# Optimization experiments

Measured on AMD Instinct MI355X. Metric: run time of the kernel, lower is better.

Reference implementation:

```python
import jax, jax.numpy as jnp
import numpy as np

DIM = 64
HID = 128
DT_MAX = 0.1
BATCH = 16384


def _lin_init(k, fi, fo):
    kw, kb = jax.random.split(k)
    s = 1.0 / np.sqrt(fi)
    w = jax.random.uniform(kw, (fi, fo), minval=-s, maxval=s, dtype=jnp.float32)
    b = jax.random.uniform(kb, (fo,), minval=-s, maxval=s, dtype=jnp.float32)
    return w, b


def setup_inputs() -> dict:
    key = jax.random.key(0)
    ks = list(jax.random.split(key, 16))
    it = iter(ks)
    inp = {"z": jax.random.normal(next(it), (BATCH, DIM), dtype=jnp.float32)}
    layouts = [
        ("H", [(DIM, HID), (HID, HID), (HID, 1)]),
        ("D", [(DIM, HID), (HID, HID), (HID, 1)]),
        ("J", [(DIM, HID), (HID, DIM * DIM)]),
        ("B", [(DIM, HID), (HID, DIM * DIM)]),
        ("u", [(DIM, HID), (HID, DIM)]),
    ]
    for name, dims in layouts:
        for li, (fi, fo) in enumerate(dims, 1):
            w, b = _lin_init(next(it), fi, fo)
            inp[f"{name}w{li}"] = w
            inp[f"{name}b{li}"] = b
    inp["dt_logit"] = jnp.zeros((), dtype=jnp.float32)
    inp["energy_target"] = jnp.asarray(1.0, dtype=jnp.float32)
    return inp


def _scalar_net(z, w1, b1, w2, b2, w3, b3):
    # Linear->SiLU->Linear->SiLU->Linear, then softplus, squeeze -> [B]
    h = jax.nn.silu(z @ w1 + b1)
    h = jax.nn.silu(h @ w2 + b2)
    return jax.nn.softplus((h @ w3 + b3)[..., 0])


def reference(z, Hw1, Hb1, Hw2, Hb2, Hw3, Hb3,
              Dw1, Db1, Dw2, Db2, Dw3, Db3,
              Jw1, Jb1, Jw2, Jb2, Bw1, Bb1, Bw2, Bb2,
              uw1, ub1, uw2, ub2, dt_logit, energy_target):
    H = _scalar_net(z, Hw1, Hb1, Hw2, Hb2, Hw3, Hb3)  # [B]
    # autograd.grad(H.sum(), z) / grad(D.sum(), z)
    gH = jax.grad(lambda zz: _scalar_net(zz, Hw1, Hb1, Hw2, Hb2, Hw3, Hb3).sum())(z)
    gD = jax.grad(lambda zz: _scalar_net(zz, Dw1, Db1, Dw2, Db2, Dw3, Db3).sum())(z)
    # skew-symmetric J
    A = (jax.nn.silu(z @ Jw1 + Jb1) @ Jw2 + Jb2).reshape(-1, DIM, DIM)
    Jm = A - jnp.swapaxes(A, 1, 2)
    # PSD R = B B^T
    Bm = (jax.nn.silu(z @ Bw1 + Bb1) @ Bw2 + Bb2).reshape(-1, DIM, DIM)
    R = jnp.einsum('bik,bjk->bij', Bm, Bm)
    cons = jnp.einsum('bij,bj->bi', Jm, gH)
    diss = -jnp.einsum('bij,bj->bi', R, gD)
    u = jnp.tanh(z @ uw1 + ub1) @ uw2 + ub2
    pump = (energy_target - H)[:, None] * u
    dt = jax.nn.sigmoid(dt_logit) * DT_MAX
    dz = cons + diss + 0.1 * pump
    return z + dt * dz
```

## Files before the change

kernel.cpp:

```cpp
#include <hip/hip_runtime.h>

#define DIM 64
#define HID 128

typedef __attribute__((ext_vector_type(8))) short short8;
typedef __attribute__((ext_vector_type(4))) float f32x4;
typedef _Float16 h16x8 __attribute__((ext_vector_type(8)));
typedef _Float16 h16x2 __attribute__((ext_vector_type(2)));
typedef unsigned short ushort_t;

#define MFMA(A, B, C) __builtin_amdgcn_mfma_f32_16x16x32_bf16((A), (B), (C), 0, 0, 0)
#define MFMAH(A, B, C) __builtin_amdgcn_mfma_f32_16x16x32_f16((A), (B), (C), 0, 0, 0)

__device__ __forceinline__ float sigm(float x) { return 1.f / (1.f + __expf(-x)); }
__device__ __forceinline__ float siluf(float x) { return x * sigm(x); }
__device__ __forceinline__ float silup(float x) { float s = sigm(x); return s + x * s * (1.f - s); }
__device__ __forceinline__ float softplusf(float x) {
    if (x > 20.f) return x;
    return log1pf(__expf(x));
}
__device__ __forceinline__ ushort_t f2bf(float f) {
    union { float f; unsigned int u; } v; v.f = f;
    unsigned int r = v.u + 0x7fffu + ((v.u >> 16) & 1u);
    return (ushort_t)(r >> 16);
}
__device__ __forceinline__ ushort_t f2h(float f) {
    _Float16 h = (_Float16)f;
    union { _Float16 h; ushort_t u; } v; v.h = h; return v.u;
}
__device__ __forceinline__ _Float16 u2h(ushort_t u) {
    union { ushort_t u; _Float16 h; } v; v.u = u; return v.h;
}

#define OFF_HW1F  0
#define OFF_HW2F  8192
#define OFF_HW2TF 24576
#define OFF_HW1TF 40960
#define OFF_DW1F  49152
#define OFF_DW2F  57344
#define OFF_DW2TF 73728
#define OFF_DW1TF 90112
#define OFF_UW1F  98304
#define OFF_UW2F  106496
#define OFF_JW1F  114688
#define OFF_BW1F  122880

extern "C" __global__ __launch_bounds__(256)
void prep3_kernel(const float* __restrict__ Jw2, const float* __restrict__ Jb2,
                  const float* __restrict__ Bw2, const float* __restrict__ Bb2,
                  const float* __restrict__ Hw1, const float* __restrict__ Hw2,
                  const float* __restrict__ Dw1, const float* __restrict__ Dw2,
                  const float* __restrict__ uw1, const float* __restrict__ uw2,
                  const float* __restrict__ Jw1, const float* __restrict__ Bw1,
                  ushort_t* __restrict__ JW, ushort_t* __restrict__ BW1, ushort_t* __restrict__ BW2,
                  ushort_t* __restrict__ JbdF, ushort_t* __restrict__ Bb2F, ushort_t* __restrict__ Bb2TF,
                  ushort_t* __restrict__ SWF)
{
    const int b = blockIdx.x;
    if (b < 6144) {
        const int m = b >> 11;
        const int o = ((b & 2047) << 8) | threadIdx.x;
        const int e = o & 7, n = (o >> 3) & 63, g = (o >> 9) & 3, kt = o >> 11;
        const int k = (kt << 5) | (g << 3) | e;
        const int oi = k >> 7, h = k & 127;
        float val;
        if (m == 0)      val = Jw2[h * 4096 + n * 64 + oi] - Jw2[h * 4096 + oi * 64 + n];
        else if (m == 1) val = Bw2[h * 4096 + oi * 64 + n];
        else             val = Bw2[h * 4096 + n * 64 + oi];
        ushort_t* dst = (m == 0) ? JW : (m == 1) ? BW1 : BW2;
        dst[o] = f2h(val);
    } else if (b == 6144) {
        for (int e0 = threadIdx.x; e0 < 12288; e0 += 256) {
            const int m = e0 >> 12, o = e0 & 4095;
            const int e = o & 7, n = (o >> 3) & 63, g = (o >> 9) & 3, kb = o >> 11;
            const int k = (kb << 5) | (g << 3) | e;
            float val; ushort_t* dst;
            if (m == 0)      { val = Jb2[n * 64 + k] - Jb2[k * 64 + n]; dst = JbdF; }
            else if (m == 1) { val = Bb2[k * 64 + n];                   dst = Bb2F; }
            else             { val = Bb2[n * 64 + k];                   dst = Bb2TF; }
            dst[o] = f2h(val);
        }
    } else {
        const int e = (b - 6145) * 256 + threadIdx.x;
        float val = 0.f;
        if (e < 98304) {
            const int net = e / 49152;
            const int o = e - net * 49152;
            const float* W1s = net ? Dw1 : Hw1;
            const float* W2s = net ? Dw2 : Hw2;
            if (o < 8192) {
                int ks = o & 31, n = (o >> 5) & 127, kt = o >> 12;
                val = W1s[(kt * 32 + ks) * 128 + n];
            } else if (o < 24576) {
                int o2 = o - 8192;
                int ks = o2 & 31, n = (o2 >> 5) & 127, kt = o2 >> 12;
                val = W2s[(kt * 32 + ks) * 128 + n];
            } else if (o < 40960) {
                int o3 = o - 24576;
                int ks = o3 & 31, n = (o3 >> 5) & 127, kt = o3 >> 12;
                val = W2s[n * 128 + kt * 32 + ks];
            } else {
                int o4 = o - 40960;
                int ks = o4 & 31, n = (o4 >> 5) & 63, kt = o4 >> 11;
                val = W1s[n * 128 + kt * 32 + ks];
            }
        } else if (e < 106496) {
            int o = e - 98304;
            int ks = o & 31, n = (o >> 5) & 127, kt = o >> 12;
            val = uw1[(kt * 32 + ks) * 128 + n];
        } else if (e < 114688) {
            int o = e - 106496;
            int ks = o & 31, n = (o >> 5) & 63, kt = o >> 11;
            val = uw2[(kt * 32 + ks) * 64 + n];
        } else if (e < 122880) {
            int o = e - 114688;
            int ks = o & 31, n = (o >> 5) & 127, kt = o >> 12;
            val = Jw1[(kt * 32 + ks) * 128 + n];
        } else {
            int o = e - 122880;
            int ks = o & 31, n = (o >> 5) & 127, kt = o >> 12;
            val = Bw1[(kt * 32 + ks) * 128 + n];
        }
        SWF[e] = f2bf(val);
    }
}

__device__ __forceinline__ void scalar_net(
    int tid, int r0,
    const ushort_t* zbp, ushort_t* S1, ushort_t* S2, ushort_t* S3,
    float* yacc, float* srow, float* Hrow,
    const ushort_t* W1f, const ushort_t* W2f, const ushort_t* W2Tf, const ushort_t* W1Tf,
    const float* B1, const float* B2, const float* W3, const float* B3,
    ushort_t* gOut, int storeH)
{
    const int lane = tid & 63, w = tid >> 6;
    const int mt = w & 1, nh = w >> 1;
    const int cl = lane & 15, qq = lane >> 4;
    const int arow = mt * 16 + cl;
    const int crow = mt * 16 + qq * 4;

    {
        short8 a0 = *(const short8*)&zbp[arow * 72 + (qq << 3)];
        short8 a1 = *(const short8*)&zbp[arow * 72 + 32 + (qq << 3)];
        #pragma unroll
        for (int nt = 0; nt < 2; ++nt) {
            int n = nh * 32 + nt * 16 + cl;
            f32x4 acc = {0.f, 0.f, 0.f, 0.f};
            short8 b0 = *(const short8*)&W1f[(n << 5) + (qq << 3)];
            short8 b1 = *(const short8*)&W1f[((128 + n) << 5) + (qq << 3)];
            acc = MFMA(a0, b0, acc); acc = MFMA(a1, b1, acc);
            float bv = B1[n];
            #pragma unroll
            for (int q = 0; q < 4; ++q) {
                float aa = acc[q] + bv;
                S1[(crow + q) * 136 + n] = f2bf(siluf(aa));
                S2[(crow + q) * 136 + n] = f2bf(silup(aa));
            }
        }
    }
    __syncthreads();
    {
        short8 a[4];
        #pragma unroll
        for (int kt = 0; kt < 4; ++kt)
            a[kt] = *(const short8*)&S1[arow * 136 + kt * 32 + (qq << 3)];
        float yp[4] = {0.f, 0.f, 0.f, 0.f};
        #pragma unroll
        for (int nt = 0; nt < 2; ++nt) {
            int n = nh * 32 + nt * 16 + cl;
            f32x4 acc = {0.f, 0.f, 0.f, 0.f};
            #pragma unroll
            for (int kt = 0; kt < 4; ++kt) {
                short8 bb = *(const short8*)&W2f[((kt * 128 + n) << 5) + (qq << 3)];
                acc = MFMA(a[kt], bb, acc);
            }
            float bv = B2[n], w3v = W3[n];
            #pragma unroll
            for (int q = 0; q < 4; ++q) {
                float a2 = acc[q] + bv;
                yp[q] += siluf(a2) * w3v;
                S3[(crow + q) * 136 + n] = f2bf(w3v * silup(a2));
            }
        }
        #pragma unroll
        for (int q = 0; q < 4; ++q) {
            float p = yp[q];
            p += __shfl_xor(p, 1); p += __shfl_xor(p, 2);
            p += __shfl_xor(p, 4); p += __shfl_xor(p, 8);
            if (cl == 0) atomicAdd(&yacc[crow + q], p);
        }
    }
    __syncthreads();
    if (tid < 32) {
        float a3 = yacc[tid] + B3[0];
        srow[tid] = sigm(a3);
        if (storeH) Hrow[tid] = softplusf(a3);
        yacc[tid] = 0.f;
    }
    __syncthreads();
    {
        short8 a[4];
        #pragma unroll
        for (int kt = 0; kt < 4; ++kt)
            a[kt] = *(const short8*)&S3[arow * 136 + kt * 32 + (qq << 3)];
        #pragma unroll
        for (int nt = 0; nt < 2; ++nt) {
            int n = nh * 32 + nt * 16 + cl;
            f32x4 acc = {0.f, 0.f, 0.f, 0.f};
            #pragma unroll
            for (int kt = 0; kt < 4; ++kt) {
                short8 bb = *(const short8*)&W2Tf[((kt * 128 + n) << 5) + (qq << 3)];
                acc = MFMA(a[kt], bb, acc);
            }
            #pragma unroll
            for (int q = 0; q < 4; ++q) {
                float sp;
                { union { unsigned int u; float f; } v;
                  v.u = ((unsigned int)S2[(crow + q) * 136 + n]) << 16; sp = v.f; }
                S1[(crow + q) * 136 + n] = f2bf(acc[q] * sp);
            }
        }
    }
    __syncthreads();
    {
        short8 a[4];
        #pragma unroll
        for (int kt = 0; kt < 4; ++kt)
            a[kt] = *(const short8*)&S1[arow * 136 + kt * 32 + (qq << 3)];
        int n = nh * 16 + cl;
        f32x4 acc = {0.f, 0.f, 0.f, 0.f};
        #pragma unroll
        for (int kt = 0; kt < 4; ++kt) {
            short8 bb = *(const short8*)&W1Tf[((kt * 64 + n) << 5) + (qq << 3)];
            acc = MFMA(a[kt], bb, acc);
        }
        #pragma unroll
        for (int q = 0; q < 4; ++q) {
            int row = crow + q;
            gOut[(size_t)(r0 + row) * 64 + n] = f2h(srow[row] * acc[q]);
        }
    }
    __syncthreads();
}

extern "C" __global__ __launch_bounds__(512, 4)
void k1_kernel(const float* __restrict__ z,
               const float* __restrict__ Hb1, const float* __restrict__ Hb2,
               const float* __restrict__ Hw3, const float* __restrict__ Hb3,
               const float* __restrict__ Db1, const float* __restrict__ Db2,
               const float* __restrict__ Dw3, const float* __restrict__ Db3,
               const float* __restrict__ ub1, const float* __restrict__ ub2,
               const float* __restrict__ dtl, const float* __restrict__ etg,
               const ushort_t* __restrict__ SWF,
               ushort_t* __restrict__ gHbf, ushort_t* __restrict__ gDbf,
               float* __restrict__ out)
{
    __shared__ __align__(16) ushort_t zb[32][72];
    __shared__ __align__(16) ushort_t S1[32][136];
    __shared__ __align__(16) ushort_t S2[32][136];
    __shared__ __align__(16) ushort_t S3[32][136];
    __shared__ float yacc[32];
    __shared__ float srow[32];
    __shared__ float Hrow[32];

    const int tid = threadIdx.x;
    const int r0 = blockIdx.x * 32;

    {
        const float4* zg = (const float4*)(z + (size_t)r0 * 64);
        float4 v = zg[tid];
        int row = tid >> 4, c4 = (tid & 15) * 4;
        zb[row][c4 + 0] = f2bf(v.x); zb[row][c4 + 1] = f2bf(v.y);
        zb[row][c4 + 2] = f2bf(v.z); zb[row][c4 + 3] = f2bf(v.w);
        if (tid < 32) yacc[tid] = 0.f;
    }
    __syncthreads();

    scalar_net(tid, r0, &zb[0][0], &S1[0][0], &S2[0][0], &S3[0][0], yacc, srow, Hrow,
               SWF + OFF_HW1F, SWF + OFF_HW2F, SWF + OFF_HW2TF, SWF + OFF_HW1TF,
               Hb1, Hb2, Hw3, Hb3, gHbf, 1);
    scalar_net(tid, r0, &zb[0][0], &S1[0][0], &S2[0][0], &S3[0][0], yacc, srow, Hrow,
               SWF + OFF_DW1F, SWF + OFF_DW2F, SWF + OFF_DW2TF, SWF + OFF_DW1TF,
               Db1, Db2, Dw3, Db3, gDbf, 0);

    const int lane = tid & 63, w = tid >> 6;
    const int mt = w & 1, nh = w >> 1;
    const int cl = lane & 15, qq = lane >> 4;
    const int arow = mt * 16 + cl;
    const int crow = mt * 16 + qq * 4;

    {
        short8 a0 = *(const short8*)&zb[arow][(qq << 3)];
        short8 a1 = *(const short8*)&zb[arow][32 + (qq << 3)];
        const ushort_t* W1f = SWF + OFF_UW1F;
        #pragma unroll
        for (int nt = 0; nt < 2; ++nt) {
            int n = nh * 32 + nt * 16 + cl;
            f32x4 acc = {0.f, 0.f, 0.f, 0.f};
            short8 b0 = *(const short8*)&W1f[(n << 5) + (qq << 3)];
            short8 b1 = *(const short8*)&W1f[((128 + n) << 5) + (qq << 3)];
            acc = MFMA(a0, b0, acc); acc = MFMA(a1, b1, acc);
            float bv = ub1[n];
            #pragma unroll
            for (int q = 0; q < 4; ++q)
                S1[crow + q][n] = f2bf(tanhf(acc[q] + bv));
        }
    }
    __syncthreads();
    {
        short8 a[4];
        #pragma unroll
        for (int kt = 0; kt < 4; ++kt)
            a[kt] = *(const short8*)&S1[arow][kt * 32 + (qq << 3)];
        const ushort_t* W2f = SWF + OFF_UW2F;
        const float dtv = 0.1f * sigm(dtl[0]);
        const float et = etg[0];
        int n = nh * 16 + cl;
        f32x4 acc = {0.f, 0.f, 0.f, 0.f};
        #pragma unroll
        for (int kt = 0; kt < 4; ++kt) {
            short8 bb = *(const short8*)&W2f[((kt * 64 + n) << 5) + (qq << 3)];
            acc = MFMA(a[kt], bb, acc);
        }
        float bv = ub2[n];
        #pragma unroll
        for (int q = 0; q < 4; ++q) {
            int row = crow + q;
            size_t idx = (size_t)(r0 + row) * 64 + n;
            out[idx] = z[idx] + dtv * 0.1f * (et - Hrow[row]) * (acc[q] + bv);
        }
    }
}

#define LOADHF2H(SRC, HA, HB)                                                     \
    do {                                                                          \
        _Pragma("unroll")                                                         \
        for (int q4 = 0; q4 < 4; ++q4) {                                          \
            short8 sa = *(const short8*)&(SRC)[rr0][q4 * 32 + (qq << 3)];         \
            short8 sb = *(const short8*)&(SRC)[rr1][q4 * 32 + (qq << 3)];         \
            _Pragma("unroll")                                                     \
            for (int e = 0; e < 4; ++e) {                                         \
                h16x2 ta, tb;                                                     \
                ta[0] = u2h((ushort_t)sa[e * 2]); ta[1] = u2h((ushort_t)sa[e * 2 + 1]); \
                tb[0] = u2h((ushort_t)sb[e * 2]); tb[1] = u2h((ushort_t)sb[e * 2 + 1]); \
                (HA)[q4 * 4 + e] = ta;                                            \
                (HB)[q4 * 4 + e] = tb;                                            \
            }                                                                     \
        }                                                                         \
    } while (0)

#define HEAVY_PASS(Wbase, BFbase, G, HA, HB, A00, A01, A10, A11)                  \
    do {                                                                          \
        _Pragma("unroll 2")                                                       \
        for (int jj = 0; jj < 32; ++jj) {                                         \
            const int j = 2 * jj + ks;                                            \
            const ushort_t* bp = (Wbase) + (size_t)j * 8192 + (qq << 9);          \
            h16x8 bf0[4], bf1[4];                                                 \
            _Pragma("unroll")                                                     \
            for (int ki = 0; ki < 4; ++ki) {                                      \
                bf0[ki] = *(const h16x8*)&bp[ki * 2048 + col0 * 8];               \
                bf1[ki] = *(const h16x8*)&bp[ki * 2048 + col1 * 8];               \
            }                                                                     \
            _Float16 gA = u2h((G)[rr0][j]);                                       \
            _Float16 gB = u2h((G)[rr1][j]);                                       \
            h16x2 gA2; gA2[0] = gA; gA2[1] = gA;                                  \
            h16x2 gB2; gB2[0] = gB; gB2[1] = gB;                                  \
            _Pragma("unroll")                                                     \
            for (int ki = 0; ki < 4; ++ki) {                                      \
                union { h16x2 h2[4]; h16x8 v; } aA, aB;                           \
                _Pragma("unroll")                                                 \
                for (int e = 0; e < 4; ++e) {                                     \
                    aA.h2[e] = (HA)[ki * 4 + e] * gA2;                            \
                    aB.h2[e] = (HB)[ki * 4 + e] * gB2;                            \
                }                                                                 \
                A00 = MFMAH(aA.v, bf0[ki], A00); A01 = MFMAH(aA.v, bf1[ki], A01); \
                A10 = MFMAH(aB.v, bf0[ki], A10); A11 = MFMAH(aB.v, bf1[ki], A11); \
            }                                                                     \
        }                                                                         \
                             \
        {                                                                         \
            h16x8 abA = *(const h16x8*)&(G)[rr0][(ks << 5) + (qq << 3)];          \
            h16x8 abB = *(const h16x8*)&(G)[rr1][(ks << 5) + (qq << 3)];          \
            const ushort_t* bpb = (BFbase) + (ks << 11) + (qq << 9);              \
            h16x8 b0 = *(const h16x8*)&bpb[col0 * 8];                             \
            h16x8 b1 = *(const h16x8*)&bpb[col1 * 8];                             \
            A00 = MFMAH(abA, b0, A00); A01 = MFMAH(abA, b1, A01);                 \
            A10 = MFMAH(abB, b0, A10); A11 = MFMAH(abB, b1, A11);                 \
        }                                                                         \
                                             \
        __syncthreads();                                                          \
        if (ks == 1) {                                                            \
            _Pragma("unroll")                                                     \
            for (int q = 0; q < 4; ++q) {                                         \
                Pb[orow0 + q][col0] = A00[q]; Pb[orow0 + q][col1] = A01[q];       \
                Pb[orow1 + q][col0] = A10[q]; Pb[orow1 + q][col1] = A11[q];       \
            }                                                                     \
        }                                                                         \
        __syncthreads();                                                          \
        if (ks == 0) {                                                            \
            _Pragma("unroll")                                                     \
            for (int q = 0; q < 4; ++q) {                                         \
                A00[q] += Pb[orow0 + q][col0]; A01[q] += Pb[orow0 + q][col1];     \
                A10[q] += Pb[orow1 + q][col0]; A11[q] += Pb[orow1 + q][col1];     \
            }                                                                     \
        }                                                                         \
        __syncthreads();                                                          \
    } while (0)

extern "C" __global__ __launch_bounds__(256, 3)
void k2_kernel(const float* __restrict__ z,
               const float* __restrict__ Jb1, const float* __restrict__ Bb1,
               const float* __restrict__ dtl,
               const ushort_t* __restrict__ JW, const ushort_t* __restrict__ BW1,
               const ushort_t* __restrict__ BW2,
               const ushort_t* __restrict__ JbdF, const ushort_t* __restrict__ Bb2F,
               const ushort_t* __restrict__ Bb2TF,
               const ushort_t* __restrict__ SWF,
               const ushort_t* __restrict__ gHbf, const ushort_t* __restrict__ gDbf,
               float* __restrict__ out)
{
    __shared__ __align__(16) ushort_t zb[32][72];
    __shared__ __align__(16) ushort_t hJ2[32][136];
    __shared__ __align__(16) ushort_t hB2[32][136];
    __shared__ __align__(16) ushort_t gHb[32][72];
    __shared__ __align__(16) ushort_t gDb[32][72];
    __shared__ __align__(16) ushort_t vb2[32][72];
    __shared__ __align__(16) float Pb[32][68];

    const int tid = threadIdx.x;
    const int r0 = blockIdx.x * 32;

    {
        const float4* zg = (const float4*)(z + (size_t)r0 * 64);
        #pragma unroll
        for (int it = 0; it < 2; ++it) {
            int i = it * 256 + tid;
            float4 v = zg[i];
            int row = i >> 4, c4 = (i & 15) * 4;
            zb[row][c4 + 0] = f2bf(v.x); zb[row][c4 + 1] = f2bf(v.y);
            zb[row][c4 + 2] = f2bf(v.z); zb[row][c4 + 3] = f2bf(v.w);
        }
        const short8* gh = (const short8*)(gHbf + (size_t)r0 * 64);
        const short8* gd = (const short8*)(gDbf + (size_t)r0 * 64);
        int row = tid >> 3, s = tid & 7;
        *(short8*)&gHb[row][s * 8] = gh[tid];
        *(short8*)&gDb[row][s * 8] = gd[tid];
    }
    __syncthreads();

    const int lane = tid & 63, w = tid >> 6;
    const int cl = lane & 15, qq = lane >> 4;
    const int mt = w & 1, nh = w >> 1;
    const int arow = mt * 16 + cl;
    const int crowL = mt * 16 + qq * 4;

    {
        short8 a0 = *(const short8*)&zb[arow][(qq << 3)];
        short8 a1 = *(const short8*)&zb[arow][32 + (qq << 3)];
        const ushort_t* JW1f = SWF + OFF_JW1F;
        const ushort_t* BW1f = SWF + OFF_BW1F;
        #pragma unroll
        for (int nt = 0; nt < 4; ++nt) {
            int n = nh * 64 + nt * 16 + cl;
            f32x4 accJ = {0.f, 0.f, 0.f, 0.f}, accB = {0.f, 0.f, 0.f, 0.f};
            short8 jb0 = *(const short8*)&JW1f[(n << 5) + (qq << 3)];
            short8 jb1 = *(const short8*)&JW1f[((128 + n) << 5) + (qq << 3)];
            accJ = MFMA(a0, jb0, accJ); accJ = MFMA(a1, jb1, accJ);
            short8 bb0 = *(const short8*)&BW1f[(n << 5) + (qq << 3)];
            short8 bb1 = *(const short8*)&BW1f[((128 + n) << 5) + (qq << 3)];
            accB = MFMA(a0, bb0, accB); accB = MFMA(a1, bb1, accB);
            float jbv = Jb1[n], bbv = Bb1[n];
            #pragma unroll
            for (int q = 0; q < 4; ++q) {
                hJ2[crowL + q][n] = f2h(siluf(accJ[q] + jbv));
                hB2[crowL + q][n] = f2h(siluf(accB[q] + bbv));
            }
        }
    }
    __syncthreads();

    const int ch = w & 1;
    const int ks = w >> 1;
    const int rr0 = cl;
    const int rr1 = cl + 16;
    const int col0 = ch * 32 + cl;
    const int col1 = col0 + 16;
    const int orow0 = qq * 4;
    const int orow1 = orow0 + 16;

    h16x2 hfJA[16], hfJB[16], hfBA[16], hfBB[16];
    f32x4 c00 = {0,0,0,0}, c01 = {0,0,0,0}, c10 = {0,0,0,0}, c11 = {0,0,0,0};
    f32x4 v00 = {0,0,0,0}, v01 = {0,0,0,0}, v10 = {0,0,0,0}, v11 = {0,0,0,0};
    f32x4 d00 = {0,0,0,0}, d01 = {0,0,0,0}, d10 = {0,0,0,0}, d11 = {0,0,0,0};

    LOADHF2H(hJ2, hfJA, hfJB);
    HEAVY_PASS(JW, JbdF, gHb, hfJA, hfJB, c00, c01, c10, c11);

    LOADHF2H(hB2, hfBA, hfBB);
    HEAVY_PASS(BW1, Bb2F, gDb, hfBA, hfBB, v00, v01, v10, v11);

    if (ks == 0) {
        #pragma unroll
        for (int q = 0; q < 4; ++q) {
            vb2[orow0 + q][col0] = f2h(v00[q]); vb2[orow0 + q][col1] = f2h(v01[q]);
            vb2[orow1 + q][col0] = f2h(v10[q]); vb2[orow1 + q][col1] = f2h(v11[q]);
        }
    }
    __syncthreads();

    HEAVY_PASS(BW2, Bb2TF, vb2, hfBA, hfBB, d00, d01, d10, d11);

    if (ks == 0) {
        const float dtv = 0.1f * sigm(dtl[0]);
        #pragma unroll
        for (int q = 0; q < 4; ++q) {
            size_t i00 = (size_t)(r0 + orow0 + q) * 64 + col0;
            size_t i01 = (size_t)(r0 + orow0 + q) * 64 + col1;
            size_t i10 = (size_t)(r0 + orow1 + q) * 64 + col0;
            size_t i11 = (size_t)(r0 + orow1 + q) * 64 + col1;
            out[i00] += dtv * (c00[q] - d00[q]);
            out[i01] += dtv * (c01[q] - d01[q]);
            out[i10] += dtv * (c10[q] - d10[q]);
            out[i11] += dtv * (c11[q] - d11[q]);
        }
    }
}

extern "C" void kernel_launch(void* const* d_in, const int* in_sizes, int n_in,
                              void* d_out, int out_size, void* d_ws, size_t ws_size,
                              hipStream_t stream) {
    const float* p[27];
    for (int i = 0; i < 27; ++i) p[i] = (const float*)d_in[i];
    ushort_t* JW    = (ushort_t*)d_ws;
    ushort_t* BW1   = JW + 524288;
    ushort_t* BW2   = BW1 + 524288;
    ushort_t* JbdF  = BW2 + 524288;
    ushort_t* Bb2F  = JbdF + 4096;
    ushort_t* Bb2TF = Bb2F + 4096;
    ushort_t* gHbf  = Bb2TF + 4096;
    ushort_t* gDbf  = gHbf + (size_t)16384 * 64;
    ushort_t* SWF   = gDbf + (size_t)16384 * 64;

    hipLaunchKernelGGL(prep3_kernel, dim3(6657), dim3(256), 0, stream,
                       p[15], p[16], p[19], p[20],
                       p[1], p[3], p[7], p[9],
                       p[21], p[23], p[13], p[17],
                       JW, BW1, BW2, JbdF, Bb2F, Bb2TF, SWF);

    const int batch = in_sizes[0] / DIM;
    hipLaunchKernelGGL(k1_kernel, dim3(batch / 32), dim3(512), 0, stream,
                       p[0],
                       p[2], p[4], p[5], p[6],
                       p[8], p[10], p[11], p[12],
                       p[22], p[24],
                       p[25], p[26],
                       SWF, gHbf, gDbf, (float*)d_out);

    hipLaunchKernelGGL(k2_kernel, dim3(batch / 32), dim3(256), 0, stream,
                       p[0], p[14], p[18], p[25],
                       JW, BW1, BW2, JbdF, Bb2F, Bb2TF, SWF,
                       gHbf, gDbf, (float*)d_out);
}
```

Baseline: 110.1 us.

## Fuse scalar-net and heavy J/B kernels into one 512-thread kernel

Merges k1 (H/D gradient nets and pump term) and k2 (J/R matrix contractions) into a single kernel. gH and gD now stay in shared memory instead of round-tripping through global workspace, and the partial output is kept in a shared buffer rather than read back from global memory. The heavy pass now runs on 512 threads: the j loop is split across a new row-partition index, and partial sums are reduced with shared-memory atomicAdd in place of the two-phase Pb reduction. The cost is a much larger shared-memory footprint per block, which may lower occupancy, plus contention from the shared atomics.

```diff
diff --git a/kernel.cpp b/kernel.cpp
--- a/kernel.cpp
+++ b/kernel.cpp
@@ -126,12 +126,12 @@
 }
 
 __device__ __forceinline__ void scalar_net(
-    int tid, int r0,
+    int tid,
     const ushort_t* zbp, ushort_t* S1, ushort_t* S2, ushort_t* S3,
     float* yacc, float* srow, float* Hrow,
     const ushort_t* W1f, const ushort_t* W2f, const ushort_t* W2Tf, const ushort_t* W1Tf,
     const float* B1, const float* B2, const float* W3, const float* B3,
-    ushort_t* gOut, int storeH)
+    ushort_t* gL, int storeH)
 {
     const int lane = tid & 63, w = tid >> 6;
     const int mt = w & 1, nh = w >> 1;
@@ -237,99 +237,10 @@
         #pragma unroll
         for (int q = 0; q < 4; ++q) {
             int row = crow + q;
-            gOut[(size_t)(r0 + row) * 64 + n] = f2h(srow[row] * acc[q]);
-        }
-    }
-    __syncthreads();
-}
-
-extern "C" __global__ __launch_bounds__(512, 4)
-void k1_kernel(const float* __restrict__ z,
-               const float* __restrict__ Hb1, const float* __restrict__ Hb2,
-               const float* __restrict__ Hw3, const float* __restrict__ Hb3,
-               const float* __restrict__ Db1, const float* __restrict__ Db2,
-               const float* __restrict__ Dw3, const float* __restrict__ Db3,
-               const float* __restrict__ ub1, const float* __restrict__ ub2,
-               const float* __restrict__ dtl, const float* __restrict__ etg,
-               const ushort_t* __restrict__ SWF,
-               ushort_t* __restrict__ gHbf, ushort_t* __restrict__ gDbf,
-               float* __restrict__ out)
-{
-    __shared__ __align__(16) ushort_t zb[32][72];
-    __shared__ __align__(16) ushort_t S1[32][136];
-    __shared__ __align__(16) ushort_t S2[32][136];
-    __shared__ __align__(16) ushort_t S3[32][136];
-    __shared__ float yacc[32];
-    __shared__ float srow[32];
-    __shared__ float Hrow[32];
-
-    const int tid = threadIdx.x;
-    const int r0 = blockIdx.x * 32;
-
-    {
-        const float4* zg = (const float4*)(z + (size_t)r0 * 64);
-        float4 v = zg[tid];
-        int row = tid >> 4, c4 = (tid & 15) * 4;
-        zb[row][c4 + 0] = f2bf(v.x); zb[row][c4 + 1] = f2bf(v.y);
-        zb[row][c4 + 2] = f2bf(v.z); zb[row][c4 + 3] = f2bf(v.w);
-        if (tid < 32) yacc[tid] = 0.f;
-    }
-    __syncthreads();
-
-    scalar_net(tid, r0, &zb[0][0], &S1[0][0], &S2[0][0], &S3[0][0], yacc, srow, Hrow,
-               SWF + OFF_HW1F, SWF + OFF_HW2F, SWF + OFF_HW2TF, SWF + OFF_HW1TF,
-               Hb1, Hb2, Hw3, Hb3, gHbf, 1);
-    scalar_net(tid, r0, &zb[0][0], &S1[0][0], &S2[0][0], &S3[0][0], yacc, srow, Hrow,
-               SWF + OFF_DW1F, SWF + OFF_DW2F, SWF + OFF_DW2TF, SWF + OFF_DW1TF,
-               Db1, Db2, Dw3, Db3, gDbf, 0);
-
-    const int lane = tid & 63, w = tid >> 6;
-    const int mt = w & 1, nh = w >> 1;
-    const int cl = lane & 15, qq = lane >> 4;
-    const int arow = mt * 16 + cl;
-    const int crow = mt * 16 + qq * 4;
-
-    {
-        short8 a0 = *(const short8*)&zb[arow][(qq << 3)];
-        short8 a1 = *(const short8*)&zb[arow][32 + (qq << 3)];
-        const ushort_t* W1f = SWF + OFF_UW1F;
-        #pragma unroll
-        for (int nt = 0; nt < 2; ++nt) {
-            int n = nh * 32 + nt * 16 + cl;
-            f32x4 acc = {0.f, 0.f, 0.f, 0.f};
-            short8 b0 = *(const short8*)&W1f[(n << 5) + (qq << 3)];
-            short8 b1 = *(const short8*)&W1f[((128 + n) << 5) + (qq << 3)];
-            acc = MFMA(a0, b0, acc); acc = MFMA(a1, b1, acc);
-            float bv = ub1[n];
-            #pragma unroll
-            for (int q = 0; q < 4; ++q)
-                S1[crow + q][n] = f2bf(tanhf(acc[q] + bv));
-        }
-    }
-    __syncthreads();
-    {
-        short8 a[4];
-        #pragma unroll
-        for (int kt = 0; kt < 4; ++kt)
-            a[kt] = *(const short8*)&S1[arow][kt * 32 + (qq << 3)];
-        const ushort_t* W2f = SWF + OFF_UW2F;
-        const float dtv = 0.1f * sigm(dtl[0]);
-        const float et = etg[0];
-        int n = nh * 16 + cl;
-        f32x4 acc = {0.f, 0.f, 0.f, 0.f};
-        #pragma unroll
-        for (int kt = 0; kt < 4; ++kt) {
-            short8 bb = *(const short8*)&W2f[((kt * 64 + n) << 5) + (qq << 3)];
-            acc = MFMA(a[kt], bb, acc);
-        }
-        float bv = ub2[n];
-        #pragma unroll
-        for (int q = 0; q < 4; ++q) {
-            int row = crow + q;
-            size_t idx = (size_t)(r0 + row) * 64 + n;
-            out[idx] = z[idx] + dtv * 0.1f * (et - Hrow[row]) * (acc[q] + bv);
-        }
-    }
+            gL[row * 72 + n] = f2h(srow[row] * acc[q]);
+        }
+    }
+    __syncthreads();
 }
 
 #define LOADHF2H(SRC, HA, HB)                                                     \
@@ -349,11 +260,16 @@
         }                                                                         \
     } while (0)
 
-#define HEAVY_PASS(Wbase, BFbase, G, HA, HB, A00, A01, A10, A11)                  \
+#define HEAVY_PASS(Wbase, BFbase, HSRC, GS)                                       \
     do {                                                                          \
+        __syncthreads();                                                          \
+        for (int e2 = tid; e2 < 32 * 68; e2 += 512) (&Pb[0][0])[e2] = 0.f;        \
+        h16x2 hf0[16], hf1[16];                                                   \
+        LOADHF2H(HSRC, hf0, hf1);                                                 \
+        f32x4 A00 = {0,0,0,0}, A01 = {0,0,0,0}, A10 = {0,0,0,0}, A11 = {0,0,0,0}; \
         _Pragma("unroll 2")                                                       \
-        for (int jj = 0; jj < 32; ++jj) {                                         \
-            const int j = 2 * jj + ks;                                            \
+        for (int jj = 0; jj < 16; ++jj) {                                         \
+            const int j = (((rp << 4) + jj) << 1) + ks;                           \
             const ushort_t* bp = (Wbase) + (size_t)j * 8192 + (qq << 9);          \
             h16x8 bf0[4], bf1[4];                                                 \
             _Pragma("unroll")                                                     \
@@ -361,8 +277,8 @@
                 bf0[ki] = *(const h16x8*)&bp[ki * 2048 + col0 * 8];               \
                 bf1[ki] = *(const h16x8*)&bp[ki * 2048 + col1 * 8];               \
             }                                                                     \
-            _Float16 gA = u2h((G)[rr0][j]);                                       \
-            _Float16 gB = u2h((G)[rr1][j]);                                       \
+            _Float16 gA = u2h((GS)[rr0 * 72 + j]);                                \
+            _Float16 gB = u2h((GS)[rr1 * 72 + j]);                                \
             h16x2 gA2; gA2[0] = gA; gA2[1] = gA;                                  \
             h16x2 gB2; gB2[0] = gB; gB2[1] = gB;                                  \
             _Pragma("unroll")                                                     \
@@ -370,89 +286,131 @@
                 union { h16x2 h2[4]; h16x8 v; } aA, aB;                           \
                 _Pragma("unroll")                                                 \
                 for (int e = 0; e < 4; ++e) {                                     \
-                    aA.h2[e] = (HA)[ki * 4 + e] * gA2;                            \
-                    aB.h2[e] = (HB)[ki * 4 + e] * gB2;                            \
+                    aA.h2[e] = hf0[ki * 4 + e] * gA2;                             \
+                    aB.h2[e] = hf1[ki * 4 + e] * gB2;                             \
                 }                                                                 \
                 A00 = MFMAH(aA.v, bf0[ki], A00); A01 = MFMAH(aA.v, bf1[ki], A01); \
                 A10 = MFMAH(aB.v, bf0[ki], A10); A11 = MFMAH(aB.v, bf1[ki], A11); \
             }                                                                     \
         }                                                                         \
-                             \
-        {                                                                         \
-            h16x8 abA = *(const h16x8*)&(G)[rr0][(ks << 5) + (qq << 3)];          \
-            h16x8 abB = *(const h16x8*)&(G)[rr1][(ks << 5) + (qq << 3)];          \
+        if (rp == 0) {                                                            \
+            h16x8 abA = *(const h16x8*)&(GS)[rr0 * 72 + (ks << 5) + (qq << 3)];   \
+            h16x8 abB = *(const h16x8*)&(GS)[rr1 * 72 + (ks << 5) + (qq << 3)];   \
             const ushort_t* bpb = (BFbase) + (ks << 11) + (qq << 9);              \
             h16x8 b0 = *(const h16x8*)&bpb[col0 * 8];                             \
             h16x8 b1 = *(const h16x8*)&bpb[col1 * 8];                             \
             A00 = MFMAH(abA, b0, A00); A01 = MFMAH(abA, b1, A01);                 \
             A10 = MFMAH(abB, b0, A10); A11 = MFMAH(abB, b1, A11);                 \
         }                                                                         \
-                                             \
         __syncthreads();                                                          \
-        if (ks == 1) {                                                            \
-            _Pragma("unroll")                                                     \
-            for (int q = 0; q < 4; ++q) {                                         \
-                Pb[orow0 + q][col0] = A00[q]; Pb[orow0 + q][col1] = A01[q];       \
-                Pb[orow1 + q][col0] = A10[q]; Pb[orow1 + q][col1] = A11[q];       \
-            }                                                                     \
-        }                                                                         \
-        __syncthreads();                                                          \
-        if (ks == 0) {                                                            \
-            _Pragma("unroll")                                                     \
-            for (int q = 0; q < 4; ++q) {                                         \
-                A00[q] += Pb[orow0 + q][col0]; A01[q] += Pb[orow0 + q][col1];     \
-                A10[q] += Pb[orow1 + q][col0]; A11[q] += Pb[orow1 + q][col1];     \
-            }                                                                     \
+        _Pragma("unroll")                                                         \
+        for (int q = 0; q < 4; ++q) {                                             \
+            atomicAdd(&Pb[orow0 + q][col0], A00[q]);                              \
+            atomicAdd(&Pb[orow0 + q][col1], A01[q]);                              \
+            atomicAdd(&Pb[orow1 + q][col0], A10[q]);                              \
+            atomicAdd(&Pb[orow1 + q][col1], A11[q]);                              \
         }                                                                         \
         __syncthreads();                                                          \
     } while (0)
 
-extern "C" __global__ __launch_bounds__(256, 3)
-void k2_kernel(const float* __restrict__ z,
+extern "C" __global__ __launch_bounds__(512, 4)
+void kf_kernel(const float* __restrict__ z,
+               const float* __restrict__ Hb1, const float* __restrict__ Hb2,
+               const float* __restrict__ Hw3, const float* __restrict__ Hb3,
+               const float* __restrict__ Db1, const float* __restrict__ Db2,
+               const float* __restrict__ Dw3, const float* __restrict__ Db3,
+               const float* __restrict__ ub1, const float* __restrict__ ub2,
                const float* __restrict__ Jb1, const float* __restrict__ Bb1,
-               const float* __restrict__ dtl,
+               const float* __restrict__ dtl, const float* __restrict__ etg,
                const ushort_t* __restrict__ JW, const ushort_t* __restrict__ BW1,
                const ushort_t* __restrict__ BW2,
                const ushort_t* __restrict__ JbdF, const ushort_t* __restrict__ Bb2F,
                const ushort_t* __restrict__ Bb2TF,
                const ushort_t* __restrict__ SWF,
-               const ushort_t* __restrict__ gHbf, const ushort_t* __restrict__ gDbf,
                float* __restrict__ out)
 {
     __shared__ __align__(16) ushort_t zb[32][72];
+    __shared__ __align__(16) ushort_t S1[32][136];
+    __shared__ __align__(16) ushort_t S2[32][136];
+    __shared__ __align__(16) ushort_t S3[32][136];
+    __shared__ float yacc[32];
+    __shared__ float srow[32];
+    __shared__ float Hrow[32];
     __shared__ __align__(16) ushort_t hJ2[32][136];
     __shared__ __align__(16) ushort_t hB2[32][136];
     __shared__ __align__(16) ushort_t gHb[32][72];
     __shared__ __align__(16) ushort_t gDb[32][72];
     __shared__ __align__(16) ushort_t vb2[32][72];
     __shared__ __align__(16) float Pb[32][68];
+    __shared__ __align__(16) float baseb[32][64];
 
     const int tid = threadIdx.x;
     const int r0 = blockIdx.x * 32;
+    const float dtv = 0.1f * sigm(dtl[0]);
 
     {
         const float4* zg = (const float4*)(z + (size_t)r0 * 64);
-        #pragma unroll
-        for (int it = 0; it < 2; ++it) {
-            int i = it * 256 + tid;
-            float4 v = zg[i];
-            int row = i >> 4, c4 = (i & 15) * 4;
-            zb[row][c4 + 0] = f2bf(v.x); zb[row][c4 + 1] = f2bf(v.y);
-            zb[row][c4 + 2] = f2bf(v.z); zb[row][c4 + 3] = f2bf(v.w);
-        }
-        const short8* gh = (const short8*)(gHbf + (size_t)r0 * 64);
-        const short8* gd = (const short8*)(gDbf + (size_t)r0 * 64);
-        int row = tid >> 3, s = tid & 7;
-        *(short8*)&gHb[row][s * 8] = gh[tid];
-        *(short8*)&gDb[row][s * 8] = gd[tid];
-    }
-    __syncthreads();
+        float4 v = zg[tid];
+        int row = tid >> 4, c4 = (tid & 15) * 4;
+        zb[row][c4 + 0] = f2bf(v.x); zb[row][c4 + 1] = f2bf(v.y);
+        zb[row][c4 + 2] = f2bf(v.z); zb[row][c4 + 3] = f2bf(v.w);
+        if (tid < 32) yacc[tid] = 0.f;
+    }
+    __syncthreads();
+
+    scalar_net(tid, &zb[0][0], &S1[0][0], &S2[0][0], &S3[0][0], yacc, srow, Hrow,
+               SWF + OFF_HW1F, SWF + OFF_HW2F, SWF + OFF_HW2TF, SWF + OFF_HW1TF,
+               Hb1, Hb2, Hw3, Hb3, &gHb[0][0], 1);
+    scalar_net(tid, &zb[0][0], &S1[0][0], &S2[0][0], &S3[0][0], yacc, srow, Hrow,
+               SWF + OFF_DW1F, SWF + OFF_DW2F, SWF + OFF_DW2TF, SWF + OFF_DW1TF,
+               Db1, Db2, Dw3, Db3, &gDb[0][0], 0);
 
     const int lane = tid & 63, w = tid >> 6;
+    const int mt = w & 1, nh = w >> 1;
     const int cl = lane & 15, qq = lane >> 4;
-    const int mt = w & 1, nh = w >> 1;
     const int arow = mt * 16 + cl;
-    const int crowL = mt * 16 + qq * 4;
+    const int crow = mt * 16 + qq * 4;
+
+    {
+        short8 a0 = *(const short8*)&zb[arow][(qq << 3)];
+        short8 a1 = *(const short8*)&zb[arow][32 + (qq << 3)];
+        const ushort_t* W1f = SWF + OFF_UW1F;
+        #pragma unroll
+        for (int nt = 0; nt < 2; ++nt) {
+            int n = nh * 32 + nt * 16 + cl;
+            f32x4 acc = {0.f, 0.f, 0.f, 0.f};
+            short8 b0 = *(const short8*)&W1f[(n << 5) + (qq << 3)];
+            short8 b1 = *(const short8*)&W1f[((128 + n) << 5) + (qq << 3)];
+            acc = MFMA(a0, b0, acc); acc = MFMA(a1, b1, acc);
+            float bv = ub1[n];
+            #pragma unroll
+            for (int q = 0; q < 4; ++q)
+                S1[crow + q][n] = f2bf(tanhf(acc[q] + bv));
+        }
+    }
+    __syncthreads();
+    {
+        short8 a[4];
+        #pragma unroll
+        for (int kt = 0; kt < 4; ++kt)
+            a[kt] = *(const short8*)&S1[arow][kt * 32 + (qq << 3)];
+        const ushort_t* W2f = SWF + OFF_UW2F;
+        const float et = etg[0];
+        int n = nh * 16 + cl;
+        f32x4 acc = {0.f, 0.f, 0.f, 0.f};
+        #pragma unroll
+        for (int kt = 0; kt < 4; ++kt) {
+            short8 bb = *(const short8*)&W2f[((kt * 64 + n) << 5) + (qq << 3)];
+            acc = MFMA(a[kt], bb, acc);
+        }
+        float bv = ub2[n];
+        #pragma unroll
+        for (int q = 0; q < 4; ++q) {
+            int row = crow + q;
+            baseb[row][n] = z[(size_t)(r0 + row) * 64 + n]
+                          + dtv * 0.1f * (et - Hrow[row]) * (acc[q] + bv);
+        }
+    }
 
     {
         short8 a0 = *(const short8*)&zb[arow][(qq << 3)];
@@ -460,8 +418,8 @@
         const ushort_t* JW1f = SWF + OFF_JW1F;
         const ushort_t* BW1f = SWF + OFF_BW1F;
         #pragma unroll
-        for (int nt = 0; nt < 4; ++nt) {
-            int n = nh * 64 + nt * 16 + cl;
+        for (int nt = 0; nt < 2; ++nt) {
+            int n = nh * 32 + nt * 16 + cl;
             f32x4 accJ = {0.f, 0.f, 0.f, 0.f}, accB = {0.f, 0.f, 0.f, 0.f};
             short8 jb0 = *(const short8*)&JW1f[(n << 5) + (qq << 3)];
             short8 jb1 = *(const short8*)&JW1f[((128 + n) << 5) + (qq << 3)];
@@ -472,15 +430,16 @@
             float jbv = Jb1[n], bbv = Bb1[n];
             #pragma unroll
             for (int q = 0; q < 4; ++q) {
-                hJ2[crowL + q][n] = f2h(siluf(accJ[q] + jbv));
-                hB2[crowL + q][n] = f2h(siluf(accB[q] + bbv));
+                hJ2[crow + q][n] = f2h(siluf(accJ[q] + jbv));
+                hB2[crow + q][n] = f2h(siluf(accB[q] + bbv));
             }
         }
     }
     __syncthreads();
 
     const int ch = w & 1;
-    const int ks = w >> 1;
+    const int ks = (w >> 1) & 1;
+    const int rp = w >> 2;
     const int rr0 = cl;
     const int rr1 = cl + 16;
     const int col0 = ch * 32 + cl;
@@ -488,41 +447,22 @@
     const int orow0 = qq * 4;
     const int orow1 = orow0 + 16;
 
-    h16x2 hfJA[16], hfJB[16], hfBA[16], hfBB[16];
-    f32x4 c00 = {0,0,0,0}, c01 = {0,0,0,0}, c10 = {0,0,0,0}, c11 = {0,0,0,0};
-    f32x4 v00 = {0,0,0,0}, v01 = {0,0,0,0}, v10 = {0,0,0,0}, v11 = {0,0,0,0};
-    f32x4 d00 = {0,0,0,0}, d01 = {0,0,0,0}, d10 = {0,0,0,0}, d11 = {0,0,0,0};
-
-    LOADHF2H(hJ2, hfJA, hfJB);
-    HEAVY_PASS(JW, JbdF, gHb, hfJA, hfJB, c00, c01, c10, c11);
-
-    LOADHF2H(hB2, hfBA, hfBB);
-    HEAVY_PASS(BW1, Bb2F, gDb, hfBA, hfBB, v00, v01, v10, v11);
-
-    if (ks == 0) {
-        #pragma unroll
-        for (int q = 0; q < 4; ++q) {
-            vb2[orow0 + q][col0] = f2h(v00[q]); vb2[orow0 + q][col1] = f2h(v01[q]);
-            vb2[orow1 + q][col0] = f2h(v10[q]); vb2[orow1 + q][col1] = f2h(v11[q]);
-        }
-    }
-    __syncthreads();
-
-    HEAVY_PASS(BW2, Bb2TF, vb2, hfBA, hfBB, d00, d01, d10, d11);
-
-    if (ks == 0) {
-        const float dtv = 0.1f * sigm(dtl[0]);
-        #pragma unroll
-        for (int q = 0; q < 4; ++q) {
-            size_t i00 = (size_t)(r0 + orow0 + q) * 64 + col0;
-            size_t i01 = (size_t)(r0 + orow0 + q) * 64 + col1;
-            size_t i10 = (size_t)(r0 + orow1 + q) * 64 + col0;
-            size_t i11 = (size_t)(r0 + orow1 + q) * 64 + col1;
-            out[i00] += dtv * (c00[q] - d00[q]);
-            out[i01] += dtv * (c01[q] - d01[q]);
-            out[i10] += dtv * (c10[q] - d10[q]);
-            out[i11] += dtv * (c11[q] - d11[q]);
-        }
+    HEAVY_PASS(JW, JbdF, hJ2, &gHb[0][0]);
+    for (int i = tid; i < 32 * 64; i += 512) {
+        int row = i >> 6, col = i & 63;
+        baseb[row][col] += dtv * Pb[row][col];
+    }
+
+    HEAVY_PASS(BW1, Bb2F, hB2, &gDb[0][0]);
+    for (int i = tid; i < 32 * 64; i += 512) {
+        int row = i >> 6, col = i & 63;
+        vb2[row][col] = f2h(Pb[row][col]);
+    }
+
+    HEAVY_PASS(BW2, Bb2TF, hB2, &vb2[0][0]);
+    for (int i = tid; i < 32 * 64; i += 512) {
+        int row = i >> 6, col = i & 63;
+        out[(size_t)(r0 + row) * 64 + col] = baseb[row][col] - dtv * Pb[row][col];
     }
 }
 
@@ -537,9 +477,7 @@
     ushort_t* JbdF  = BW2 + 524288;
     ushort_t* Bb2F  = JbdF + 4096;
     ushort_t* Bb2TF = Bb2F + 4096;
-    ushort_t* gHbf  = Bb2TF + 4096;
-    ushort_t* gDbf  = gHbf + (size_t)16384 * 64;
-    ushort_t* SWF   = gDbf + (size_t)16384 * 64;
+    ushort_t* SWF   = Bb2TF + 4096;
 
     hipLaunchKernelGGL(prep3_kernel, dim3(6657), dim3(256), 0, stream,
                        p[15], p[16], p[19], p[20],
@@ -548,16 +486,13 @@
                        JW, BW1, BW2, JbdF, Bb2F, Bb2TF, SWF);
 
     const int batch = in_sizes[0] / DIM;
-    hipLaunchKernelGGL(k1_kernel, dim3(batch / 32), dim3(512), 0, stream,
+    hipLaunchKernelGGL(kf_kernel, dim3(batch / 32), dim3(512), 0, stream,
                        p[0],
                        p[2], p[4], p[5], p[6],
                        p[8], p[10], p[11], p[12],
                        p[22], p[24],
+                       p[14], p[18],
                        p[25], p[26],
-                       SWF, gHbf, gDbf, (float*)d_out);
-
-    hipLaunchKernelGGL(k2_kernel, dim3(batch / 32), dim3(256), 0, stream,
-                       p[0], p[14], p[18], p[25],
                        JW, BW1, BW2, JbdF, Bb2F, Bb2TF, SWF,
-                       gHbf, gDbf, (float*)d_out);
-}
+                       (float*)d_out);
+}
```

After: 183.2 us. 1.66x slower.
